# Kernel optimization log

Measured on AMD Instinct MI355X. Metric: run time of the kernel, lower is better.

## Reference

```python
import jax, jax.numpy as jnp
import numpy as np

C, Q, R, N, S = 10, 1000, 1024, 512, 10000
ALPHA, GAMMA, DIST_W, EPS_EYE = 0.25, 2.0, 0.1, 1e-4


def setup_inputs() -> dict:
    key = jax.random.key(0)
    ks = jax.random.split(key, 8)
    box_features = jax.random.normal(ks[0], (N, R), jnp.float32)
    id_labels = jax.random.randint(ks[1], (N,), 0, C, dtype=jnp.int32)
    id_data = jax.random.normal(ks[2], (C, Q, R), jnp.float32)
    id_data_counter = jnp.full((C,), Q, dtype=jnp.int32)  # full queues -> VOS path enabled
    W_pred = jax.random.normal(ks[3], (C, R), jnp.float32) * 0.02
    b_pred = jnp.zeros((C,), jnp.float32)
    w_e = jax.random.uniform(ks[4], (C, 1), jnp.float32)  # energy_score_weights ~ U[0,1)
    dist_W1 = jax.random.normal(ks[5], (512, 1), jnp.float32) * 0.5
    dist_b1 = jnp.zeros((512,), jnp.float32)
    dist_W2 = jax.random.normal(ks[6], (1, 512), jnp.float32) * 0.05
    dist_b2 = jnp.zeros((1,), jnp.float32)
    eps = jax.random.normal(ks[7], (C, S, R), jnp.float32)  # standard-normal draws for rsample
    return dict(box_features=box_features, id_labels=id_labels, id_data=id_data,
                id_data_counter=id_data_counter, W_pred=W_pred, b_pred=b_pred, w_e=w_e,
                dist_W1=dist_W1, dist_b1=dist_b1, dist_W2=dist_W2, dist_b2=dist_b2, eps=eps)


def _bce_logits(x, y):
    # binary_cross_entropy_with_logits, elementwise
    return jnp.maximum(x, 0.0) - x * y + jnp.log1p(jnp.exp(-jnp.abs(x)))


def _queue_update(id_data, counter, labels, feats):
    # Faithful sequential per-sample queue scatter (torch Python loop) as lax.scan.
    def step(carry, inp):
        data, cnt = carry
        lab, f = inp
        c = cnt[lab]
        row = data[lab]                                            # [Q,R]
        row_set = jax.lax.dynamic_update_slice(row, f[None], (c, 0))
        row_roll = jnp.concatenate([row[1:], f[None]], axis=0)     # drop oldest, append
        full = c >= row.shape[0]
        new_row = jnp.where(full, row_roll, row_set)
        data = data.at[lab].set(new_row)
        cnt = cnt.at[lab].add(jnp.where(full, 0, 1))
        return (data, cnt), None
    (data, cnt), _ = jax.lax.scan(step, (id_data, counter), (labels, feats))
    return data, cnt


def _energy(x, w_e):
    # m + log(exp(x-m) @ relu(w_e)); all classes valid (counter > 0)
    m = jnp.max(x, axis=1, keepdims=True)
    return m + jnp.log(jnp.exp(x - m) @ jax.nn.relu(w_e))


def reference(box_features, id_labels, id_data, id_data_counter, W_pred, b_pred, w_e,
              dist_W1, dist_b1, dist_W2, dist_b2, eps):
    scores = box_features @ W_pred.T + b_pred                      # [N,C]
    # ---- classification: sigmoid focal loss (sum / num_pos) ----
    t = jax.nn.one_hot(id_labels, C, dtype=scores.dtype)
    p = jax.nn.sigmoid(scores)
    ce = _bce_logits(scores, t)
    p_t = p * t + (1.0 - p) * (1.0 - t)
    alpha_t = ALPHA * t + (1.0 - ALPHA) * (1.0 - t)
    cls_loss = jnp.sum(alpha_t * ce * (1.0 - p_t) ** GAMMA) / scores.shape[0]
    # ---- per-class queue scatter (detached features) ----
    data, _ = _queue_update(id_data, id_data_counter, id_labels,
                            jax.lax.stop_gradient(box_features))
    # ---- class Gaussians: per-class mean, shared covariance ----
    mu = jnp.mean(data, axis=1)                                    # [C,R]
    x_tilda = (data - mu[:, None, :]).reshape(-1, R)               # all classes valid (full queues)
    sigma = x_tilda.T @ x_tilda / x_tilda.shape[0] + EPS_EYE * jnp.eye(R, dtype=data.dtype)
    L = jnp.linalg.cholesky(sigma)                                 # [R,R]
    # ---- VOS: rsample 10000 per class, keep lowest-density (top-1 of -log_prob) ----
    # samples = mu + eps @ L.T ; log_prob = const - 0.5*||eps||^2, so argmin density = argmax ||eps||^2
    sq = jnp.sum(eps * eps, axis=-1)                               # [C,S]
    idx = jnp.argmax(sq, axis=-1)                                  # [C]
    eps_sel = jnp.take_along_axis(eps, idx[:, None, None], axis=1)[:, 0, :]  # [C,R]
    vos_samples = mu + eps_sel @ L.T                               # [C,R]
    scores_vos = vos_samples @ W_pred.T + b_pred                   # [C,C]
    # ---- dist loss: energy score -> tiny MLP -> BCE, weight 0.1 ----
    e_all = jnp.concatenate([_energy(scores, w_e), _energy(scores_vos, w_e)], axis=0)  # [N+C,1]
    h = jax.nn.relu(e_all @ dist_W1.T + dist_b1)
    logits = (h @ dist_W2.T + dist_b2)[:, 0]                       # [N+C]
    y = jnp.concatenate([jnp.ones((scores.shape[0],), logits.dtype),
                         jnp.zeros((C,), logits.dtype)])
    dist_loss = DIST_W * jnp.mean(_bce_logits(logits, y))
    return cls_loss, dist_loss
```

## Files before the change

kernel.cpp:

```cpp
#include <hip/hip_runtime.h>
#include <hip/hip_cooperative_groups.h>
#include <stdint.h>

namespace cg = cooperative_groups;

#define C_ 10
#define Q_ 1000
#define R_ 1024
#define N_ 512
#define S_ 10000
#define CQ 10000
#define KP 10240
#define SPLITK 8
#define GRIDC 105

#define OFF_DT    0ULL
#define OFF_GP    20971520ULL
#define OFF_SIG   54525952ULL
#define OFF_MU    58720256ULL
#define OFF_E     58761216ULL
#define OFF_CLS   58763304ULL
#define OFF_AMAX  58763312ULL
#define OFF_KC    58763392ULL
#define OFF_GOFF  58763432ULL
#define OFF_GIDX  58763472ULL

typedef __attribute__((ext_vector_type(8))) short bf16x8;
typedef __attribute__((ext_vector_type(4))) float f32x4;

__global__ void k_prep(const int* __restrict__ labels, int* kc, int* goff, int* gidx,
                       float* mu, float* cls_accum, unsigned long long* amax) {
  __shared__ int cnt[C_];
  __shared__ int off[C_];
  int t = threadIdx.x;
  if (t < C_) cnt[t] = 0;
  __syncthreads();
  for (int i = t; i < N_; i += 256) atomicAdd(&cnt[labels[i]], 1);
  __syncthreads();
  if (t == 0) {
    int acc = 0;
    for (int c = 0; c < C_; c++) { off[c] = acc; goff[c] = acc; kc[c] = cnt[c]; acc += cnt[c]; }
    for (int i = 0; i < N_; i++) { int c = labels[i]; gidx[off[c]++] = i; }
    *cls_accum = 0.f;
  }
  if (t < C_) amax[t] = 0ULL;
  for (int i = t; i < C_ * R_; i += 256) mu[i] = 0.f;
}

__global__ __launch_bounds__(256) void k_epsmax(const float* __restrict__ eps,
                                                unsigned long long* amax) {
  int c = blockIdx.y;
  int chunk = blockIdx.x;
  int t = threadIdx.x, lane = t & 63, w = t >> 6;
  const int per = 79;
  int s0 = chunk * per;
  int s1 = min(s0 + per, S_);
  float bv = -1.f; int bs = 0;
  for (int s = s0 + w; s < s1; s += 4) {
    const float4* p = (const float4*)(eps + ((size_t)c * S_ + s) * R_);
    float acc = 0.f;
#pragma unroll
    for (int m = 0; m < 4; m++) {
      float4 v = p[lane + 64 * m];
      acc += v.x * v.x + v.y * v.y + v.z * v.z + v.w * v.w;
    }
#pragma unroll
    for (int d = 32; d > 0; d >>= 1) acc += __shfl_xor(acc, d);
    if (acc > bv) { bv = acc; bs = s; }
  }
  __shared__ float svv[4]; __shared__ int ssi[4];
  if (lane == 0) { svv[w] = bv; ssi[w] = bs; }
  __syncthreads();
  if (t == 0) {
    float m = svv[0]; int mi = ssi[0];
    for (int i = 1; i < 4; i++) if (svv[i] > m) { m = svv[i]; mi = ssi[i]; }
    if (m >= 0.f) {
      unsigned long long pk = ((unsigned long long)__float_as_uint(m) << 32) | (unsigned)mi;
      atomicMax(amax + c, pk);
    }
  }
}

__global__ void k_scores(const float* __restrict__ box, const int* __restrict__ labels,
                         const float* __restrict__ Wp, const float* __restrict__ bp,
                         const float* __restrict__ we, float* __restrict__ E,
                         float* cls_accum) {
  int i = blockIdx.x;
  int lane = threadIdx.x;
  float s[C_];
#pragma unroll
  for (int k = 0; k < C_; k++) s[k] = 0.f;
  const float* bi = box + (size_t)i * R_;
  for (int r = lane; r < R_; r += 64) {
    float x = bi[r];
#pragma unroll
    for (int k = 0; k < C_; k++) s[k] += x * Wp[k * R_ + r];
  }
#pragma unroll
  for (int k = 0; k < C_; k++) {
#pragma unroll
    for (int d = 32; d > 0; d >>= 1) s[k] += __shfl_xor(s[k], d);
  }
  if (lane == 0) {
    int lab = labels[i];
    float sc[C_]; float m = -1e30f;
#pragma unroll
    for (int k = 0; k < C_; k++) { sc[k] = s[k] + bp[k]; m = fmaxf(m, sc[k]); }
    float fsum = 0.f, esum = 0.f;
#pragma unroll
    for (int k = 0; k < C_; k++) {
      float x = sc[k];
      float tt = (k == lab) ? 1.f : 0.f;
      float p = 1.f / (1.f + expf(-x));
      float ce = fmaxf(x, 0.f) - x * tt + log1pf(expf(-fabsf(x)));
      float pt = p * tt + (1.f - p) * (1.f - tt);
      float at = 0.25f * tt + 0.75f * (1.f - tt);
      float om = 1.f - pt;
      fsum += at * ce * om * om;
      esum += expf(x - m) * fmaxf(we[k], 0.f);
    }
    atomicAdd(cls_accum, fsum);
    E[i] = m + logf(esum);
  }
}

__global__ __launch_bounds__(256) void k_convert(const float* __restrict__ idd,
                                                 const float* __restrict__ box,
                                                 const int* __restrict__ kc,
                                                 const int* __restrict__ goff,
                                                 const int* __restrict__ gidx,
                                                 uint16_t* __restrict__ Dt,
                                                 float* __restrict__ mu) {
  __shared__ const float* rowsrc[64];
  __shared__ int rcls[64];
  __shared__ float T[64][65];
  int bk = blockIdx.x;
  int br = blockIdx.y;
  int t = threadIdx.x;
  int t0 = bk * 64, r0 = br * 64;
  if (t < 64) {
    int row = t0 + t;
    const float* src = nullptr; int c = -1;
    if (row < CQ) {
      c = row / Q_;
      int q = row - c * Q_;
      int k = kc[c];
      if (q < Q_ - k) src = idd + (size_t)(c * Q_ + q + k) * R_;
      else            src = box + (size_t)gidx[goff[c] + (q - (Q_ - k))] * R_;
    }
    rowsrc[t] = src; rcls[t] = c;
  }
  __syncthreads();
  int rr = t & 63, k4 = t >> 6;
#pragma unroll
  for (int it = 0; it < 16; it++) {
    int kk = k4 + it * 4;
    const float* src = rowsrc[kk];
    T[kk][rr] = src ? src[r0 + rr] : 0.f;
  }
  __syncthreads();
  if (t < 64 && t0 < CQ) {
    int c0 = rcls[0];
    float s0 = 0.f, s1 = 0.f; int c1 = -1;
    for (int kk = 0; kk < 64; kk++) {
      int c = rcls[kk]; float v = T[kk][t];
      if (c == c0) s0 += v; else if (c >= 0) { c1 = c; s1 += v; }
    }
    atomicAdd(&mu[c0 * R_ + r0 + t], s0);
    if (c1 >= 0) atomicAdd(&mu[c1 * R_ + r0 + t], s1);
  }
  int kk2 = t & 63, r4 = t >> 6;
#pragma unroll
  for (int it = 0; it < 16; it++) {
    int rr2 = r4 + it * 4;
    float v = T[kk2][rr2];
    uint32_t u = __float_as_uint(v);
    uint32_t b = (u + 0x7fffu + ((u >> 16) & 1u)) >> 16;
    Dt[(size_t)(r0 + rr2) * KP + t0 + kk2] = (uint16_t)b;
  }
}

__global__ __launch_bounds__(256) void k_gemm(const uint16_t* __restrict__ Dt,
                                              float* __restrict__ GP) {
  __shared__ __align__(16) uint16_t lA[2][8192];
  __shared__ __align__(16) uint16_t lB[2][8192];
  int bi = blockIdx.x, bj = blockIdx.y, bz = blockIdx.z;
  int t = threadIdx.x;
  int lane = t & 63, w = t >> 6;
  int i0 = bi * 128, j0 = bj * 128;
  int lane16 = lane & 15, quad = lane >> 4;
  int wm = w >> 1, wn = w & 1;
  int row = t >> 1, half = t & 1;
  int kz = bz * 1280;
  const uint16_t* ga = Dt + (size_t)(i0 + row) * KP + kz + half * 32;
  const uint16_t* gb = Dt + (size_t)(j0 + row) * KP + kz + half * 32;
  int swz[4];
#pragma unroll
  for (int u = 0; u < 4; u++) swz[u] = (((half << 2) | u) ^ (row & 7)) << 3;
  int x7 = lane16 & 7;

  f32x4 acc[4][4];
#pragma unroll
  for (int a = 0; a < 4; a++)
#pragma unroll
    for (int b = 0; b < 4; b++) acc[a][b] = (f32x4){0.f, 0.f, 0.f, 0.f};

  uint4 ra[4], rb[4];
#pragma unroll
  for (int u = 0; u < 4; u++) {
    ra[u] = *(const uint4*)(ga + u * 8);
    rb[u] = *(const uint4*)(gb + u * 8);
  }
#pragma unroll
  for (int u = 0; u < 4; u++) {
    *(uint4*)(lA[0] + row * 64 + swz[u]) = ra[u];
    *(uint4*)(lB[0] + row * 64 + swz[u]) = rb[u];
  }
  __syncthreads();

  for (int it = 0; it < 20; it++) {
    int cur = it & 1;
    bool more = (it + 1) < 20;
    if (more) {
      const uint16_t* pa = ga + (it + 1) * 64;
      const uint16_t* pb = gb + (it + 1) * 64;
#pragma unroll
      for (int u = 0; u < 4; u++) {
        ra[u] = *(const uint4*)(pa + u * 8);
        rb[u] = *(const uint4*)(pb + u * 8);
      }
    }
#pragma unroll
    for (int ch = 0; ch < 2; ch++) {
      bf16x8 af[4], bfr[4];
#pragma unroll
      for (int mi = 0; mi < 4; mi++) {
        int r = wm * 64 + mi * 16 + lane16;
        int ck = ((ch << 2) | quad) ^ x7;
        af[mi] = *(const bf16x8*)(lA[cur] + r * 64 + ck * 8);
      }
#pragma unroll
      for (int ni = 0; ni < 4; ni++) {
        int r = wn * 64 + ni * 16 + lane16;
        int ck = ((ch << 2) | quad) ^ x7;
        bfr[ni] = *(const bf16x8*)(lB[cur] + r * 64 + ck * 8);
      }
#pragma unroll
      for (int mi = 0; mi < 4; mi++)
#pragma unroll
        for (int ni = 0; ni < 4; ni++)
          acc[mi][ni] = __builtin_amdgcn_mfma_f32_16x16x32_bf16(af[mi], bfr[ni], acc[mi][ni], 0, 0, 0);
    }
    if (more) {
      int nxt = cur ^ 1;
#pragma unroll
      for (int u = 0; u < 4; u++) {
        *(uint4*)(lA[nxt] + row * 64 + swz[u]) = ra[u];
        *(uint4*)(lB[nxt] + row * 64 + swz[u]) = rb[u];
      }
    }
    __syncthreads();
  }
  float* gp = GP + (size_t)bz * 1048576;
#pragma unroll
  for (int mi = 0; mi < 4; mi++)
#pragma unroll
    for (int ni = 0; ni < 4; ni++) {
      int col = j0 + wn * 64 + ni * 16 + lane16;
      int rowb = i0 + wm * 64 + mi * 16 + quad * 4;
#pragma unroll
      for (int r = 0; r < 4; r++)
        gp[(size_t)(rowb + r) * 1024 + col] = acc[mi][ni][r];
    }
}

__global__ void k_reduce(const float* __restrict__ GP, const float* __restrict__ mu,
                         float* __restrict__ sig) {
  int idx = blockIdx.x * 256 + threadIdx.x;
  int i = idx >> 10, j = idx & 1023;
  float g = 0.f;
#pragma unroll
  for (int s2 = 0; s2 < SPLITK; s2++) g += GP[idx + s2 * 1048576];
  float mm = 0.f;
#pragma unroll
  for (int c = 0; c < C_; c++) mm += mu[c * R_ + i] * mu[c * R_ + j];
  sig[idx] = g * 1e-4f - mm * 1e-7f + ((i == j) ? 1e-4f : 0.f);
}

#define AIDX(i, j) (((i) << 7) + (((j) + (i)) & 127))
__device__ void chol_diag_body(float* __restrict__ sig, int p, float* __restrict__ a) {
  int t = threadIdx.x;
  int base = p * 128;
  int lane = t & 63, wv = t >> 6;
  for (int idx = t; idx < 16384; idx += 256) {
    int i = idx >> 7, j = idx & 127;
    a[AIDX(i, j)] = sig[(size_t)(base + i) * 1024 + base + j];
  }
  __syncthreads();
  for (int panel = 0; panel < 8; panel++) {
    int j0 = panel * 16;
    if (wv == 0) {
      float pa0[16], pa1[16];
#pragma unroll
      for (int jj = 0; jj < 16; jj++) {
        pa0[jj] = a[AIDX(lane, j0 + jj)];
        pa1[jj] = a[AIDX(lane + 64, j0 + jj)];
      }
#pragma unroll
      for (int jj = 0; jj < 16; jj++) {
        int j = j0 + jj;
        float pv0 = __shfl(pa0[jj], j & 63);
        float pv1 = __shfl(pa1[jj], j & 63);
        float pv = (j < 64) ? pv0 : pv1;
// ... 40 lines not shown
          for (int n = 0; n < 4; n++) ak[n] = a[AIDX(gk + n, j0 + jj)];
#pragma unroll
          for (int m = 0; m < 4; m++)
#pragma unroll
            for (int n = 0; n < 4; n++) acc[m][n] += ai[m] * ak[n];
        }
#pragma unroll
        for (int m = 0; m < 4; m++)
#pragma unroll
          for (int n = 0; n < 4; n++)
            a[AIDX(gi + m, gk + n)] -= acc[m][n];
      }
    }
    __syncthreads();
  }
  for (int idx = t; idx < 16384; idx += 256) {
    int i = idx >> 7, j = idx & 127;
    sig[(size_t)(base + i) * 1024 + base + j] = a[AIDX(i, j)];
  }
}

#define XIDX(j, r) (((j) << 6) + (((r) + (j)) & 63))
__device__ void chol_trsm_body(float* __restrict__ sig, int p, int bid, float* __restrict__ smem) {
  float* Ls = smem;
  float* XT = smem + 8192;
  int t = threadIdx.x;
  int base = p * 128;
  int row0 = base + 128 + bid * 64;
  int r = t & 63, wv = t >> 6;
  for (int idx = t; idx < 8128; idx += 256) {
    int k = (int)((sqrtf(8.f * idx + 1.f) + 1.f) * 0.5f);
    while (k * (k - 1) / 2 > idx) k--;
    while ((k + 1) * k / 2 <= idx) k++;
    int j = idx - k * (k - 1) / 2;
    Ls[idx] = sig[(size_t)(base + k) * 1024 + base + j];
  }
  for (int idx = t; idx < 8192; idx += 256) {
    int rr = idx >> 7, j = idx & 127;
    XT[XIDX(j, rr)] = sig[(size_t)(row0 + rr) * 1024 + base + j];
  }
  float rd0 = 0.f, rd1 = 0.f;
  if (wv == 0) {
    rd0 = 1.0f / sig[(size_t)(base + r) * 1024 + base + r];
    rd1 = 1.0f / sig[(size_t)(base + 64 + r) * 1024 + base + 64 + r];
  }
  __syncthreads();
  for (int pb = 0; pb < 8; pb++) {
    int j0 = pb * 16;
    if (j0 > 0) {
      int c0 = j0 + wv * 4;
      int b0 = c0 * (c0 - 1) / 2, b1 = (c0 + 1) * c0 / 2;
      int b2 = (c0 + 2) * (c0 + 1) / 2, b3 = (c0 + 3) * (c0 + 2) / 2;
      float acc0 = 0.f, acc1 = 0.f, acc2 = 0.f, acc3 = 0.f;
      for (int k = 0; k < j0; k++) {
        float xk = XT[XIDX(k, r)];
        acc0 += xk * Ls[b0 + k];
        acc1 += xk * Ls[b1 + k];
        acc2 += xk * Ls[b2 + k];
        acc3 += xk * Ls[b3 + k];
      }
      XT[XIDX(c0 + 0, r)] -= acc0;
      XT[XIDX(c0 + 1, r)] -= acc1;
      XT[XIDX(c0 + 2, r)] -= acc2;
      XT[XIDX(c0 + 3, r)] -= acc3;
    }
    __syncthreads();
    if (wv == 0) {
#pragma unroll
      for (int jj = 0; jj < 16; jj++) {
        int j = j0 + jj;
        float rdj = (j < 64) ? __shfl(rd0, j & 63) : __shfl(rd1, j & 63);
        float xj = XT[XIDX(j, r)] * rdj;
        XT[XIDX(j, r)] = xj;
#pragma unroll
        for (int kk = jj + 1; kk < 16; kk++) {
          int k2 = j0 + kk;
          XT[XIDX(k2, r)] -= xj * Ls[k2 * (k2 - 1) / 2 + j];
        }
      }
    }
    __syncthreads();
  }
  for (int idx = t; idx < 8192; idx += 256) {
    int rr = idx >> 7, j = idx & 127;
    sig[(size_t)(row0 + rr) * 1024 + base + j] = XT[XIDX(j, rr)];
  }
}

__device__ void chol_syrk_body(float* __restrict__ sig, int p, int bid, float* __restrict__ smem) {
  float (*PA)[65] = (float(*)[65])smem;
  float (*PB)[65] = (float(*)[65])(smem + 4160);
  int t = threadIdx.x;
  int tb = p * 128 + 128;
  int I = 0;
  while ((I + 1) * (I + 2) / 2 <= bid) I++;
  int K = bid - I * (I + 1) / 2;
  int gi = tb + I * 64, gk = tb + K * 64;
  int a4 = t >> 4, b4 = t & 15;
  float acc[4][4];
#pragma unroll
  for (int m = 0; m < 4; m++)
#pragma unroll
    for (int n = 0; n < 4; n++) acc[m][n] = 0.f;
  for (int ch = 0; ch < 2; ch++) {
    int cb = p * 128 + ch * 64;
    for (int idx = t; idx < 4096; idx += 256) {
      int rr = idx >> 6, cc = idx & 63;
      PA[rr][cc] = sig[(size_t)(gi + rr) * 1024 + cb + cc];
      PB[rr][cc] = sig[(size_t)(gk + rr) * 1024 + cb + cc];
    }
    __syncthreads();
    for (int j = 0; j < 64; j++) {
      float pa[4], pb[4];
#pragma unroll
      for (int m = 0; m < 4; m++) pa[m] = PA[a4 * 4 + m][j];
#pragma unroll
      for (int n = 0; n < 4; n++) pb[n] = PB[b4 * 4 + n][j];
#pragma unroll
      for (int m = 0; m < 4; m++)
#pragma unroll
        for (int n = 0; n < 4; n++) acc[m][n] += pa[m] * pb[n];
    }
    __syncthreads();
  }
#pragma unroll
  for (int m = 0; m < 4; m++)
#pragma unroll
    for (int n = 0; n < 4; n++)
      sig[(size_t)(gi + a4 * 4 + m) * 1024 + gk + b4 * 4 + n] -= acc[m][n];
}

__device__ void vos_body(const float* __restrict__ eps, const float* __restrict__ L,
                         const float* __restrict__ mu, const float* __restrict__ Wp,
                         const float* __restrict__ bp, const float* __restrict__ we,
                         const unsigned long long* __restrict__ amax,
                         float* __restrict__ E, int c, float* __restrict__ smem) {
  float* es = smem;
  float* ys = smem + 1024;
  float* sv = smem + 2048;
  int t = threadIdx.x;
  int idx = (int)(amax[c] & 0xffffffffULL);
  for (int i = t; i < 1024; i += 256) es[i] = eps[((size_t)c * S_ + idx) * R_ + i];
  __syncthreads();
  for (int rep = 0; rep < 4; rep++) {
    int i = rep * 256 + t;
    const float* Lr = L + (size_t)i * 1024;
    float a0 = 0.f, a1 = 0.f, a2 = 0.f, a3 = 0.f;
    int j = 0;
    for (; j + 3 <= i; j += 4) {
      a0 += es[j] * Lr[j];
      a1 += es[j + 1] * Lr[j + 1];
      a2 += es[j + 2] * Lr[j + 2];
      a3 += es[j + 3] * Lr[j + 3];
    }
    for (; j <= i; j++) a0 += es[j] * Lr[j];
    ys[i] = mu[c * R_ + i] * 1e-3f + ((a0 + a1) + (a2 + a3));
  }
  __syncthreads();
  if (t < C_) {
    float acc = bp[t];
    const float* Wr = Wp + (size_t)t * R_;
    for (int j = 0; j < 1024; j++) acc += ys[j] * Wr[j];
    sv[t] = acc;
  }
  __syncthreads();
  if (t == 0) {
    float m = -1e30f;
    for (int k = 0; k < C_; k++) m = fmaxf(m, sv[k]);
    float sum = 0.f;
    for (int k = 0; k < C_; k++) sum += expf(sv[k] - m) * fmaxf(we[k], 0.f);
    E[N_ + c] = m + logf(sum);
  }
}

__device__ void dist_body(const float* __restrict__ E, const float* __restrict__ W1,
                          const float* __restrict__ b1, const float* __restrict__ W2,
                          const float* __restrict__ b2, const float* __restrict__ cls_accum,
                          float* __restrict__ out, float* __restrict__ smem) {
  float* sW1 = smem;
  float* sb1 = smem + 512;
  float* sW2 = smem + 1024;
  float* red = smem + 1536;
  int t = threadIdx.x;
  for (int i = t; i < 512; i += 256) { sW1[i] = W1[i]; sb1[i] = b1[i]; sW2[i] = W2[i]; }
  __syncthreads();
  float sum = 0.f;
  for (int i = t; i < N_ + C_; i += 256) {
    float e = E[i];
    float acc = b2[0];
    for (int j = 0; j < 512; j++) acc += sW2[j] * fmaxf(e * sW1[j] + sb1[j], 0.f);
    float y = (i < N_) ? 1.f : 0.f;
    float l = fmaxf(acc, 0.f) - acc * y + log1pf(expf(-fabsf(acc)));
    sum += l;
  }
#pragma unroll
  for (int d = 32; d > 0; d >>= 1) sum += __shfl_xor(sum, d);
  if ((t & 63) == 0) red[t >> 6] = sum;
  __syncthreads();
  if (t == 0) {
    out[1] = 0.1f * (red[0] + red[1] + red[2] + red[3]) / 522.f;
    out[0] = *cls_accum / 512.f;
  }
}

__global__ __launch_bounds__(256) void k_chol(float* __restrict__ sig,
    const float* __restrict__ eps, const float* __restrict__ mu,
    const float* __restrict__ Wp, const float* __restrict__ bp,
    const float* __restrict__ we, const unsigned long long* __restrict__ amax,
    float* __restrict__ E, const float* __restrict__ W1, const float* __restrict__ b1,
    const float* __restrict__ W2, const float* __restrict__ b2,
    const float* __restrict__ cls_accum, float* __restrict__ out) {
  cg::grid_group grid = cg::this_grid();
  __shared__ __align__(16) float smem[16384];
  int bid = blockIdx.x;
  for (int p = 0; p < 8; p++) {
    if (bid == 0) chol_diag_body(sig, p, smem);
    __threadfence(); grid.sync();
    int rows = 1024 - 128 * (p + 1);
    if (rows > 0) {
      int nb = rows >> 6;
      if (bid < nb) chol_trsm_body(sig, p, bid, smem);
      __threadfence(); grid.sync();
      int nt = nb * (nb + 1) / 2;
      for (int bx = bid; bx < nt; bx += GRIDC) chol_syrk_body(sig, p, bx, smem);
      __threadfence(); grid.sync();
    }
  }
  if (bid < C_) vos_body(eps, sig, mu, Wp, bp, we, amax, E, bid, smem);
  __threadfence(); grid.sync();
  if (bid == 0) dist_body(E, W1, b1, W2, b2, cls_accum, out, smem);
}

extern "C" void kernel_launch(void* const* d_in, const int* in_sizes, int n_in,
                              void* d_out, int out_size, void* d_ws, size_t ws_size,
                              hipStream_t stream) {
  (void)in_sizes; (void)n_in; (void)out_size; (void)ws_size;
  const float* box  = (const float*)d_in[0];
  const int*   lab  = (const int*)d_in[1];
  const float* idd  = (const float*)d_in[2];
  const float* Wp   = (const float*)d_in[4];
  const float* bp   = (const float*)d_in[5];
  const float* we   = (const float*)d_in[6];
  const float* W1   = (const float*)d_in[7];
  const float* b1   = (const float*)d_in[8];
  const float* W2   = (const float*)d_in[9];
  const float* b2   = (const float*)d_in[10];
  const float* eps  = (const float*)d_in[11];
  float* out = (float*)d_out;

  char* ws = (char*)d_ws;
  uint16_t* Dt = (uint16_t*)(ws + OFF_DT);
  float* GP    = (float*)(ws + OFF_GP);
  float* sig   = (float*)(ws + OFF_SIG);
  float* mu    = (float*)(ws + OFF_MU);
  float* E     = (float*)(ws + OFF_E);
  float* clsa  = (float*)(ws + OFF_CLS);
  unsigned long long* amax = (unsigned long long*)(ws + OFF_AMAX);
  int* kc   = (int*)(ws + OFF_KC);
  int* goff = (int*)(ws + OFF_GOFF);
  int* gidx = (int*)(ws + OFF_GIDX);

  hipLaunchKernelGGL(k_prep, dim3(1), dim3(256), 0, stream, lab, kc, goff, gidx, mu, clsa, amax);
  hipLaunchKernelGGL(k_epsmax, dim3(127, C_), dim3(256), 0, stream, eps, amax);
  hipLaunchKernelGGL(k_scores, dim3(N_), dim3(64), 0, stream, box, lab, Wp, bp, we, E, clsa);
  hipLaunchKernelGGL(k_convert, dim3(160, 16), dim3(256), 0, stream, idd, box, kc, goff, gidx, Dt, mu);
  hipLaunchKernelGGL(k_gemm, dim3(8, 8, SPLITK), dim3(256), 0, stream, Dt, GP);
  hipLaunchKernelGGL(k_reduce, dim3(4096), dim3(256), 0, stream, GP, mu, sig);
  {
    float* a0 = sig; const float* a1 = eps; const float* a2 = mu; const float* a3 = Wp;
    const float* a4 = bp; const float* a5 = we; const unsigned long long* a6 = amax;
    float* a7 = E; const float* a8 = W1; const float* a9 = b1; const float* a10 = W2;
    const float* a11 = b2; const float* a12 = clsa; float* a13 = out;
    void* args[] = {&a0, &a1, &a2, &a3, &a4, &a5, &a6, &a7, &a8, &a9, &a10, &a11, &a12, &a13};
    hipLaunchCooperativeKernel(k_chol, dim3(GRIDC), dim3(256), args, 0, stream);
  }
}
```

Measured before the change: 2.515 ms.

## Replace cooperative Cholesky with per-panel launches and fuse front-end kernels

Merges the prep, eps argmax, score and convert kernels into one launch, with a memset taking over the zero-initialisation. The cooperative Cholesky with grid syncs is replaced by per-panel fused TRSM+SYRK launches. The last-arriving block, detected via an atomic counter, factors the next diagonal block, and the first diagonal factor is triggered from the GEMM. The split-K reduction and covariance correction are folded lazily into the Cholesky reads, and VOS plus the distance loss become one kernel that uses a last-block pattern. This removes grid-wide barriers and several launches, but adds redundant per-block label scans and recomputation of triangular solves per tile.

Result: slower. 3.081 ms (+22.5%).

```diff
diff --git a/kernel.cpp b/kernel.cpp
--- a/kernel.cpp
+++ b/kernel.cpp
@@ -1,8 +1,5 @@
 #include <hip/hip_runtime.h>
-#include <hip/hip_cooperative_groups.h>
 #include <stdint.h>
-
-namespace cg = cooperative_groups;
 
 #define C_ 10
 #define Q_ 1000
@@ -12,7 +9,7 @@
 #define CQ 10000
 #define KP 10240
 #define SPLITK 8
-#define GRIDC 105
+#define GPN 1048576
 
 #define OFF_DT    0ULL
 #define OFF_GP    20971520ULL
@@ -21,132 +18,127 @@
 #define OFF_E     58761216ULL
 #define OFF_CLS   58763304ULL
 #define OFF_AMAX  58763312ULL
-#define OFF_KC    58763392ULL
-#define OFF_GOFF  58763432ULL
-#define OFF_GIDX  58763472ULL
+#define OFF_CNT   58763392ULL
+#define ZERO_BYTES 43200ULL
 
 typedef __attribute__((ext_vector_type(8))) short bf16x8;
 typedef __attribute__((ext_vector_type(4))) float f32x4;
 
-__global__ void k_prep(const int* __restrict__ labels, int* kc, int* goff, int* gidx,
-                       float* mu, float* cls_accum, unsigned long long* amax) {
-  __shared__ int cnt[C_];
-  __shared__ int off[C_];
-  int t = threadIdx.x;
-  if (t < C_) cnt[t] = 0;
-  __syncthreads();
-  for (int i = t; i < N_; i += 256) atomicAdd(&cnt[labels[i]], 1);
-  __syncthreads();
-  if (t == 0) {
-    int acc = 0;
-    for (int c = 0; c < C_; c++) { off[c] = acc; goff[c] = acc; kc[c] = cnt[c]; acc += cnt[c]; }
-    for (int i = 0; i < N_; i++) { int c = labels[i]; gidx[off[c]++] = i; }
-    *cls_accum = 0.f;
-  }
-  if (t < C_) amax[t] = 0ULL;
-  for (int i = t; i < C_ * R_; i += 256) mu[i] = 0.f;
-}
-
-__global__ __launch_bounds__(256) void k_epsmax(const float* __restrict__ eps,
-                                                unsigned long long* amax) {
-  int c = blockIdx.y;
-  int chunk = blockIdx.x;
-  int t = threadIdx.x, lane = t & 63, w = t >> 6;
-  const int per = 79;
-  int s0 = chunk * per;
-  int s1 = min(s0 + per, S_);
-  float bv = -1.f; int bs = 0;
-  for (int s = s0 + w; s < s1; s += 4) {
-    const float4* p = (const float4*)(eps + ((size_t)c * S_ + s) * R_);
-    float acc = 0.f;
-#pragma unroll
-    for (int m = 0; m < 4; m++) {
-      float4 v = p[lane + 64 * m];
-      acc += v.x * v.x + v.y * v.y + v.z * v.z + v.w * v.w;
-    }
-#pragma unroll
-    for (int d = 32; d > 0; d >>= 1) acc += __shfl_xor(acc, d);
-    if (acc > bv) { bv = acc; bs = s; }
-  }
-  __shared__ float svv[4]; __shared__ int ssi[4];
-  if (lane == 0) { svv[w] = bv; ssi[w] = bs; }
-  __syncthreads();
-  if (t == 0) {
-    float m = svv[0]; int mi = ssi[0];
-    for (int i = 1; i < 4; i++) if (svv[i] > m) { m = svv[i]; mi = ssi[i]; }
-    if (m >= 0.f) {
-      unsigned long long pk = ((unsigned long long)__float_as_uint(m) << 32) | (unsigned)mi;
-      atomicMax(amax + c, pk);
-    }
-  }
-}
-
-__global__ void k_scores(const float* __restrict__ box, const int* __restrict__ labels,
-                         const float* __restrict__ Wp, const float* __restrict__ bp,
-                         const float* __restrict__ we, float* __restrict__ E,
-                         float* cls_accum) {
-  int i = blockIdx.x;
-  int lane = threadIdx.x;
-  float s[C_];
-#pragma unroll
-  for (int k = 0; k < C_; k++) s[k] = 0.f;
-  const float* bi = box + (size_t)i * R_;
-  for (int r = lane; r < R_; r += 64) {
-    float x = bi[r];
-#pragma unroll
-    for (int k = 0; k < C_; k++) s[k] += x * Wp[k * R_ + r];
-  }
-#pragma unroll
-  for (int k = 0; k < C_; k++) {
-#pragma unroll
-    for (int d = 32; d > 0; d >>= 1) s[k] += __shfl_xor(s[k], d);
-  }
-  if (lane == 0) {
-    int lab = labels[i];
-    float sc[C_]; float m = -1e30f;
-#pragma unroll
-    for (int k = 0; k < C_; k++) { sc[k] = s[k] + bp[k]; m = fmaxf(m, sc[k]); }
-    float fsum = 0.f, esum = 0.f;
-#pragma unroll
-    for (int k = 0; k < C_; k++) {
-      float x = sc[k];
-      float tt = (k == lab) ? 1.f : 0.f;
-      float p = 1.f / (1.f + expf(-x));
-      float ce = fmaxf(x, 0.f) - x * tt + log1pf(expf(-fabsf(x)));
-      float pt = p * tt + (1.f - p) * (1.f - tt);
-      float at = 0.25f * tt + 0.75f * (1.f - tt);
-      float om = 1.f - pt;
-      fsum += at * ce * om * om;
-      esum += expf(x - m) * fmaxf(we[k], 0.f);
-    }
-    atomicAdd(cls_accum, fsum);
-    E[i] = m + logf(esum);
-  }
-}
-
-__global__ __launch_bounds__(256) void k_convert(const float* __restrict__ idd,
-                                                 const float* __restrict__ box,
-                                                 const int* __restrict__ kc,
-                                                 const int* __restrict__ goff,
-                                                 const int* __restrict__ gidx,
-                                                 uint16_t* __restrict__ Dt,
-                                                 float* __restrict__ mu) {
+#define AIDX(i, j) (((i) << 7) + (((j) + (i)) & 127))
+#define XIDX(j, r) (((j) << 6) + (((r) + (j)) & 63))
+
+__global__ __launch_bounds__(256) void k_front(
+    const float* __restrict__ box, const int* __restrict__ labels,
+    const float* __restrict__ idd, const float* __restrict__ Wp,
+    const float* __restrict__ bp, const float* __restrict__ we,
+    const float* __restrict__ eps, uint16_t* __restrict__ Dt,
+    float* __restrict__ mu, float* __restrict__ E, float* cls_accum,
+    unsigned long long* amax) {
   __shared__ const float* rowsrc[64];
   __shared__ int rcls[64];
   __shared__ float T[64][65];
-  int bk = blockIdx.x;
-  int br = blockIdx.y;
+  __shared__ int s_cnt[C_];
+  __shared__ float svv[4];
+  __shared__ int ssi[4];
+  int b = blockIdx.x;
   int t = threadIdx.x;
+
+  if (b < 1270) {
+    int c = b / 127, chunk = b % 127;
+    int lane = t & 63, w = t >> 6;
+    const int per = 79;
+    int s0 = chunk * per;
+    int s1 = min(s0 + per, S_);
+    float bv = -1.f; int bs = 0;
+    for (int s = s0 + w; s < s1; s += 4) {
+      const float4* p = (const float4*)(eps + ((size_t)c * S_ + s) * R_);
+      float acc = 0.f;
+#pragma unroll
+      for (int m = 0; m < 4; m++) {
+        float4 v = p[lane + 64 * m];
+        acc += v.x * v.x + v.y * v.y + v.z * v.z + v.w * v.w;
+      }
+#pragma unroll
+      for (int d = 32; d > 0; d >>= 1) acc += __shfl_xor(acc, d);
+      if (acc > bv) { bv = acc; bs = s; }
+    }
+    if (lane == 0) { svv[w] = bv; ssi[w] = bs; }
+    __syncthreads();
+    if (t == 0) {
+      float m = svv[0]; int mi = ssi[0];
+      for (int i = 1; i < 4; i++) if (svv[i] > m) { m = svv[i]; mi = ssi[i]; }
+      if (m >= 0.f) {
+        unsigned long long pk = ((unsigned long long)__float_as_uint(m) << 32) | (unsigned)mi;
+        atomicMax(amax + c, pk);
+      }
+    }
+    return;
+  }
+
+  if (b < 1270 + 128) {
+    int lane = t & 63, wv = t >> 6;
+    int i = (b - 1270) * 4 + wv;
+    float s[C_];
+#pragma unroll
+    for (int k = 0; k < C_; k++) s[k] = 0.f;
+    const float* bi = box + (size_t)i * R_;
+    for (int r = lane; r < R_; r += 64) {
+      float x = bi[r];
+#pragma unroll
+      for (int k = 0; k < C_; k++) s[k] += x * Wp[k * R_ + r];
+    }
+#pragma unroll
+    for (int k = 0; k < C_; k++) {
+#pragma unroll
+      for (int d = 32; d > 0; d >>= 1) s[k] += __shfl_xor(s[k], d);
+    }
+    if (lane == 0) {
+      int lab = labels[i];
+      float sc[C_]; float m = -1e30f;
+#pragma unroll
+      for (int k = 0; k < C_; k++) { sc[k] = s[k] + bp[k]; m = fmaxf(m, sc[k]); }
+      float fsum = 0.f, esum = 0.f;
+#pragma unroll
+      for (int k = 0; k < C_; k++) {
+        float x = sc[k];
+        float tt = (k == lab) ? 1.f : 0.f;
+        float p = 1.f / (1.f + expf(-x));
+        float ce = fmaxf(x, 0.f) - x * tt + log1pf(expf(-fabsf(x)));
+        float pt = p * tt + (1.f - p) * (1.f - tt);
+        float at = 0.25f * tt + 0.75f * (1.f - tt);
+        float om = 1.f - pt;
+        fsum += at * ce * om * om;
+        esum += expf(x - m) * fmaxf(we[k], 0.f);
+      }
+      atomicAdd(cls_accum, fsum);
+      E[i] = m + logf(esum);
+    }
+    return;
+  }
+
+  int cb = b - 1398;
+  int bk = cb % 160, br = cb / 160;
   int t0 = bk * 64, r0 = br * 64;
+  if (t < C_) s_cnt[t] = 0;
+  __syncthreads();
+  for (int i = t; i < N_; i += 256) atomicAdd(&s_cnt[labels[i]], 1);
+  __syncthreads();
   if (t < 64) {
     int row = t0 + t;
     const float* src = nullptr; int c = -1;
     if (row < CQ) {
       c = row / Q_;
       int q = row - c * Q_;
-      int k = kc[c];
+      int k = s_cnt[c];
       if (q < Q_ - k) src = idd + (size_t)(c * Q_ + q + k) * R_;
-      else            src = box + (size_t)gidx[goff[c] + (q - (Q_ - k))] * R_;
+      else {
+        int m = q - (Q_ - k);
+        int cnt2 = 0, gi2 = 0;
+        for (int i2 = 0; i2 < N_; i2++) {
+          if (labels[i2] == c) { if (cnt2 == m) { gi2 = i2; break; } cnt2++; }
+        }
+        src = box + (size_t)gi2 * R_;
+      }
     }
     rowsrc[t] = src; rcls[t] = c;
   }
@@ -175,128 +167,14 @@
     int rr2 = r4 + it * 4;
     float v = T[kk2][rr2];
     uint32_t u = __float_as_uint(v);
-    uint32_t b = (u + 0x7fffu + ((u >> 16) & 1u)) >> 16;
-    Dt[(size_t)(r0 + rr2) * KP + t0 + kk2] = (uint16_t)b;
-  }
-}
-
-__global__ __launch_bounds__(256) void k_gemm(const uint16_t* __restrict__ Dt,
-                                              float* __restrict__ GP) {
-  __shared__ __align__(16) uint16_t lA[2][8192];
-  __shared__ __align__(16) uint16_t lB[2][8192];
-  int bi = blockIdx.x, bj = blockIdx.y, bz = blockIdx.z;
+    uint32_t bb = (u + 0x7fffu + ((u >> 16) & 1u)) >> 16;
+    Dt[(size_t)(r0 + rr2) * KP + t0 + kk2] = (uint16_t)bb;
+  }
+}
+
+__device__ void diag_factor(float* __restrict__ a) {
   int t = threadIdx.x;
-  int lane = t & 63, w = t >> 6;
-  int i0 = bi * 128, j0 = bj * 128;
-  int lane16 = lane & 15, quad = lane >> 4;
-  int wm = w >> 1, wn = w & 1;
-  int row = t >> 1, half = t & 1;
-  int kz = bz * 1280;
-  const uint16_t* ga = Dt + (size_t)(i0 + row) * KP + kz + half * 32;
-  const uint16_t* gb = Dt + (size_t)(j0 + row) * KP + kz + half * 32;
-  int swz[4];
-#pragma unroll
-  for (int u = 0; u < 4; u++) swz[u] = (((half << 2) | u) ^ (row & 7)) << 3;
-  int x7 = lane16 & 7;
-
-  f32x4 acc[4][4];
-#pragma unroll
-  for (int a = 0; a < 4; a++)
-#pragma unroll
-    for (int b = 0; b < 4; b++) acc[a][b] = (f32x4){0.f, 0.f, 0.f, 0.f};
-
-  uint4 ra[4], rb[4];
-#pragma unroll
-  for (int u = 0; u < 4; u++) {
-    ra[u] = *(const uint4*)(ga + u * 8);
-    rb[u] = *(const uint4*)(gb + u * 8);
-  }
-#pragma unroll
-  for (int u = 0; u < 4; u++) {
-    *(uint4*)(lA[0] + row * 64 + swz[u]) = ra[u];
-    *(uint4*)(lB[0] + row * 64 + swz[u]) = rb[u];
-  }
-  __syncthreads();
-
-  for (int it = 0; it < 20; it++) {
-    int cur = it & 1;
-    bool more = (it + 1) < 20;
-    if (more) {
-      const uint16_t* pa = ga + (it + 1) * 64;
-      const uint16_t* pb = gb + (it + 1) * 64;
-#pragma unroll
-      for (int u = 0; u < 4; u++) {
-        ra[u] = *(const uint4*)(pa + u * 8);
-        rb[u] = *(const uint4*)(pb + u * 8);
-      }
-    }
-#pragma unroll
-    for (int ch = 0; ch < 2; ch++) {
-      bf16x8 af[4], bfr[4];
-#pragma unroll
-      for (int mi = 0; mi < 4; mi++) {
-        int r = wm * 64 + mi * 16 + lane16;
-        int ck = ((ch << 2) | quad) ^ x7;
-        af[mi] = *(const bf16x8*)(lA[cur] + r * 64 + ck * 8);
-      }
-#pragma unroll
-      for (int ni = 0; ni < 4; ni++) {
-        int r = wn * 64 + ni * 16 + lane16;
-        int ck = ((ch << 2) | quad) ^ x7;
-        bfr[ni] = *(const bf16x8*)(lB[cur] + r * 64 + ck * 8);
-      }
-#pragma unroll
-      for (int mi = 0; mi < 4; mi++)
-#pragma unroll
-        for (int ni = 0; ni < 4; ni++)
-          acc[mi][ni] = __builtin_amdgcn_mfma_f32_16x16x32_bf16(af[mi], bfr[ni], acc[mi][ni], 0, 0, 0);
-    }
-    if (more) {
-      int nxt = cur ^ 1;
-#pragma unroll
-      for (int u = 0; u < 4; u++) {
-        *(uint4*)(lA[nxt] + row * 64 + swz[u]) = ra[u];
-        *(uint4*)(lB[nxt] + row * 64 + swz[u]) = rb[u];
-      }
-    }
-    __syncthreads();
-  }
-  float* gp = GP + (size_t)bz * 1048576;
-#pragma unroll
-  for (int mi = 0; mi < 4; mi++)
-#pragma unroll
-    for (int ni = 0; ni < 4; ni++) {
-      int col = j0 + wn * 64 + ni * 16 + lane16;
-      int rowb = i0 + wm * 64 + mi * 16 + quad * 4;
-#pragma unroll
-      for (int r = 0; r < 4; r++)
-        gp[(size_t)(rowb + r) * 1024 + col] = acc[mi][ni][r];
-    }
-}
-
-__global__ void k_reduce(const float* __restrict__ GP, const float* __restrict__ mu,
-                         float* __restrict__ sig) {
-  int idx = blockIdx.x * 256 + threadIdx.x;
-  int i = idx >> 10, j = idx & 1023;
-  float g = 0.f;
-#pragma unroll
-  for (int s2 = 0; s2 < SPLITK; s2++) g += GP[idx + s2 * 1048576];
-  float mm = 0.f;
-#pragma unroll
-  for (int c = 0; c < C_; c++) mm += mu[c * R_ + i] * mu[c * R_ + j];
-  sig[idx] = g * 1e-4f - mm * 1e-7f + ((i == j) ? 1e-4f : 0.f);
-}
-
-#define AIDX(i, j) (((i) << 7) + (((j) + (i)) & 127))
-__device__ void chol_diag_body(float* __restrict__ sig, int p, float* __restrict__ a) {
-  int t = threadIdx.x;
-  int base = p * 128;
   int lane = t & 63, wv = t >> 6;
-  for (int idx = t; idx < 16384; idx += 256) {
-    int i = idx >> 7, j = idx & 127;
-    a[AIDX(i, j)] = sig[(size_t)(base + i) * 1024 + base + j];
-  }
-  __syncthreads();
   for (int panel = 0; panel < 8; panel++) {
     int j0 = panel * 16;
     if (wv == 0) {
@@ -367,147 +245,317 @@
     }
     __syncthreads();
   }
+}
+
+__device__ __forceinline__ float sig_corr(const float* __restrict__ GP,
+                                          const float* __restrict__ mu,
+                                          int i, int j) {
+  size_t o = (size_t)i * 1024 + j;
+  float g = 0.f;
+#pragma unroll
+  for (int s = 0; s < SPLITK; s++) g += GP[(size_t)s * GPN + o];
+  float mm = 0.f;
+#pragma unroll
+  for (int c = 0; c < C_; c++) mm += mu[c * R_ + i] * mu[c * R_ + j];
+  return g * 1e-4f - mm * 1e-7f + ((i == j) ? 1e-4f : 0.f);
+}
+
+__device__ void diag_tail(float* __restrict__ sig, const float* __restrict__ GP,
+                          const float* __restrict__ mu, int p, int fromGP,
+                          float* __restrict__ a) {
+  int t = threadIdx.x;
+  int base = p * 128;
+  for (int idx = t; idx < 16384; idx += 256) {
+    int i = idx >> 7, j = idx & 127;
+    float v = 0.f;
+    if (j <= i) {
+      if (fromGP) v = sig_corr(GP, mu, base + i, base + j);
+      else        v = sig[(size_t)(base + i) * 1024 + base + j];
+    }
+    a[AIDX(i, j)] = v;
+  }
+  __syncthreads();
+  diag_factor(a);
   for (int idx = t; idx < 16384; idx += 256) {
     int i = idx >> 7, j = idx & 127;
     sig[(size_t)(base + i) * 1024 + base + j] = a[AIDX(i, j)];
   }
 }
 
-#define XIDX(j, r) (((j) << 6) + (((r) + (j)) & 63))
-__device__ void chol_trsm_body(float* __restrict__ sig, int p, int bid, float* __restrict__ smem) {
-  float* Ls = smem;
-  float* XT = smem + 8192;
+__device__ void solve_panel(const float* __restrict__ sig, const float* __restrict__ GP,
+                            const float* __restrict__ mu, int base, int grow,
+                            int fromGP, float* __restrict__ XT, float rd0, float rd1) {
+  int t = threadIdx.x;
+  int r = t & 63, wv = t >> 6;
+  for (int idx = t; idx < 8192; idx += 256) {
+    int rr = idx >> 7, j = idx & 127;
+    int gi = grow + rr, gj = base + j;
+    float v;
+    if (fromGP) v = sig_corr(GP, mu, gi, gj);
+    else        v = sig[(size_t)gi * 1024 + gj];
+    XT[XIDX(j, rr)] = v;
+  }
+  __syncthreads();
+  const float* L00 = sig + (size_t)base * 1024 + base;
+  for (int pb = 0; pb < 8; pb++) {
+    int j0 = pb * 16;
+    if (j0 > 0) {
+      int c0 = j0 + wv * 4;
+      const float* l0 = L00 + (size_t)c0 * 1024;
+      float acc0 = 0.f, acc1 = 0.f, acc2 = 0.f, acc3 = 0.f;
+      for (int k = 0; k < j0; k++) {
+        float xk = XT[XIDX(k, r)];
+        acc0 += xk * l0[k];
+        acc1 += xk * l0[1024 + k];
+        acc2 += xk * l0[2048 + k];
+        acc3 += xk * l0[3072 + k];
+      }
+      XT[XIDX(c0 + 0, r)] -= acc0;
+      XT[XIDX(c0 + 1, r)] -= acc1;
+      XT[XIDX(c0 + 2, r)] -= acc2;
+      XT[XIDX(c0 + 3, r)] -= acc3;
+    }
+    __syncthreads();
+    if (wv == 0) {
+#pragma unroll
+      for (int jj = 0; jj < 16; jj++) {
+        int j = j0 + jj;
+        float rdj = (j < 64) ? __shfl(rd0, j) : __shfl(rd1, j - 64);
+        float xj = XT[XIDX(j, r)] * rdj;
+        XT[XIDX(j, r)] = xj;
+#pragma unroll
+        for (int kk = jj + 1; kk < 16; kk++) {
+          int k2 = j0 + kk;
+          XT[XIDX(k2, r)] -= xj * L00[(size_t)k2 * 1024 + j];
+        }
+      }
+    }
+    __syncthreads();
+  }
+}
+
+__global__ __launch_bounds__(256) void k_gemm(const uint16_t* __restrict__ Dt,
+                                              float* __restrict__ GP,
+                                              const float* __restrict__ mu,
+                                              float* __restrict__ sig,
+                                              int* __restrict__ cnt) {
+  __shared__ __align__(16) union SM {
+    struct { uint16_t A[2][8192]; uint16_t B[2][8192]; } g;
+    float a[16384];
+  } sm;
+  int bi = blockIdx.x, bj = blockIdx.y, bz = blockIdx.z;
+  int t = threadIdx.x;
+  int lane = t & 63, w = t >> 6;
+  int i0 = bi * 128, j0 = bj * 128;
+  int lane16 = lane & 15, quad = lane >> 4;
+  int wm = w >> 1, wn = w & 1;
+  int row = t >> 1, half = t & 1;
+  int kz = bz * 1280;
+  const uint16_t* ga = Dt + (size_t)(i0 + row) * KP + kz + half * 32;
+  const uint16_t* gb = Dt + (size_t)(j0 + row) * KP + kz + half * 32;
+  int swz[4];
+#pragma unroll
+  for (int u = 0; u < 4; u++) swz[u] = (((half << 2) | u) ^ (row & 7)) << 3;
+  int x7 = lane16 & 7;
+
+  f32x4 acc[4][4];
+#pragma unroll
+  for (int a = 0; a < 4; a++)
+#pragma unroll
+    for (int b = 0; b < 4; b++) acc[a][b] = (f32x4){0.f, 0.f, 0.f, 0.f};
+
+  uint4 ra[4], rb[4];
+#pragma unroll
+  for (int u = 0; u < 4; u++) {
+    ra[u] = *(const uint4*)(ga + u * 8);
+    rb[u] = *(const uint4*)(gb + u * 8);
+  }
+#pragma unroll
+  for (int u = 0; u < 4; u++) {
+    *(uint4*)(sm.g.A[0] + row * 64 + swz[u]) = ra[u];
+    *(uint4*)(sm.g.B[0] + row * 64 + swz[u]) = rb[u];
+  }
+  __syncthreads();
+
+  for (int it = 0; it < 20; it++) {
+    int cur = it & 1;
+    bool more = (it + 1) < 20;
+    if (more) {
+      const uint16_t* pa = ga + (it + 1) * 64;
+      const uint16_t* pb = gb + (it + 1) * 64;
+#pragma unroll
+      for (int u = 0; u < 4; u++) {
+        ra[u] = *(const uint4*)(pa + u * 8);
+        rb[u] = *(const uint4*)(pb + u * 8);
+      }
+    }
+#pragma unroll
+    for (int ch = 0; ch < 2; ch++) {
+      bf16x8 af[4], bfr[4];
+#pragma unroll
+      for (int mi = 0; mi < 4; mi++) {
+        int rr = wm * 64 + mi * 16 + lane16;
+        int ck = ((ch << 2) | quad) ^ x7;
+        af[mi] = *(const bf16x8*)(sm.g.A[cur] + rr * 64 + ck * 8);
+      }
+#pragma unroll
+      for (int ni = 0; ni < 4; ni++) {
+        int rr = wn * 64 + ni * 16 + lane16;
+        int ck = ((ch << 2) | quad) ^ x7;
+        bfr[ni] = *(const bf16x8*)(sm.g.B[cur] + rr * 64 + ck * 8);
+      }
+#pragma unroll
+      for (int mi = 0; mi < 4; mi++)
+#pragma unroll
+        for (int ni = 0; ni < 4; ni++)
+          acc[mi][ni] = __builtin_amdgcn_mfma_f32_16x16x32_bf16(af[mi], bfr[ni], acc[mi][ni], 0, 0, 0);
+    }
+    if (more) {
+      int nxt = cur ^ 1;
+#pragma unroll
+      for (int u = 0; u < 4; u++) {
+        *(uint4*)(sm.g.A[nxt] + row * 64 + swz[u]) = ra[u];
+        *(uint4*)(sm.g.B[nxt] + row * 64 + swz[u]) = rb[u];
+      }
+    }
+    __syncthreads();
+  }
+  float* gp = GP + (size_t)bz * GPN;
+#pragma unroll
+  for (int mi = 0; mi < 4; mi++)
+#pragma unroll
+    for (int ni = 0; ni < 4; ni++) {
+      int col = j0 + wn * 64 + ni * 16 + lane16;
+      int rowb = i0 + wm * 64 + mi * 16 + quad * 4;
+#pragma unroll
+      for (int r = 0; r < 4; r++)
+        gp[(size_t)(rowb + r) * 1024 + col] = acc[mi][ni][r];
+    }
+  __syncthreads();
+  if (t == 0) {
+    __threadfence();
+    int d = atomicAdd(&cnt[8], 1);
+    sm.a[0] = (d == 511) ? 1.f : 0.f;
+  }
+  __syncthreads();
+  bool last = (sm.a[0] != 0.f);
+  __syncthreads();
+  if (!last) return;
+  __threadfence();
+  diag_tail(sig, GP, mu, 0, 1, sm.a);
+}
+
+__global__ __launch_bounds__(256) void k_tsyrk(float* __restrict__ sig,
+                                               float* __restrict__ GP,
+                                               const float* __restrict__ mu,
+                                               int* __restrict__ cnt,
+                                               int p, int nt) {
+  __shared__ __align__(16) float arena[16384];
+  float* XI = arena;
+  float* XK = arena + 8192;
   int t = threadIdx.x;
   int base = p * 128;
-  int row0 = base + 128 + bid * 64;
+  int bid = blockIdx.x;
+  int I = 0;
+  while ((I + 1) * (I + 2) / 2 <= bid) I++;
+  int K = bid - I * (I + 1) / 2;
+  int gi = base + 128 + I * 64, gk = base + 128 + K * 64;
   int r = t & 63, wv = t >> 6;
-  for (int idx = t; idx < 8128; idx += 256) {
-    int k = (int)((sqrtf(8.f * idx + 1.f) + 1.f) * 0.5f);
-    while (k * (k - 1) / 2 > idx) k--;
-    while ((k + 1) * k / 2 <= idx) k++;
-    int j = idx - k * (k - 1) / 2;
-    Ls[idx] = sig[(size_t)(base + k) * 1024 + base + j];
-  }
-  for (int idx = t; idx < 8192; idx += 256) {
-    int rr = idx >> 7, j = idx & 127;
-    XT[XIDX(j, rr)] = sig[(size_t)(row0 + rr) * 1024 + base + j];
-  }
   float rd0 = 0.f, rd1 = 0.f;
   if (wv == 0) {
     rd0 = 1.0f / sig[(size_t)(base + r) * 1024 + base + r];
     rd1 = 1.0f / sig[(size_t)(base + 64 + r) * 1024 + base + 64 + r];
   }
-  __syncthreads();
-  for (int pb = 0; pb < 8; pb++) {
-    int j0 = pb * 16;
-    if (j0 > 0) {
-      int c0 = j0 + wv * 4;
-      int b0 = c0 * (c0 - 1) / 2, b1 = (c0 + 1) * c0 / 2;
-      int b2 = (c0 + 2) * (c0 + 1) / 2, b3 = (c0 + 3) * (c0 + 2) / 2;
-      float acc0 = 0.f, acc1 = 0.f, acc2 = 0.f, acc3 = 0.f;
-      for (int k = 0; k < j0; k++) {
-        float xk = XT[XIDX(k, r)];
-        acc0 += xk * Ls[b0 + k];
-        acc1 += xk * Ls[b1 + k];
-        acc2 += xk * Ls[b2 + k];
-        acc3 += xk * Ls[b3 + k];
-      }
-      XT[XIDX(c0 + 0, r)] -= acc0;
-      XT[XIDX(c0 + 1, r)] -= acc1;
-      XT[XIDX(c0 + 2, r)] -= acc2;
-      XT[XIDX(c0 + 3, r)] -= acc3;
-    }
-    __syncthreads();
-    if (wv == 0) {
-#pragma unroll
-      for (int jj = 0; jj < 16; jj++) {
-        int j = j0 + jj;
-        float rdj = (j < 64) ? __shfl(rd0, j & 63) : __shfl(rd1, j & 63);
-        float xj = XT[XIDX(j, r)] * rdj;
-        XT[XIDX(j, r)] = xj;
-#pragma unroll
-        for (int kk = jj + 1; kk < 16; kk++) {
-          int k2 = j0 + kk;
-          XT[XIDX(k2, r)] -= xj * Ls[k2 * (k2 - 1) / 2 + j];
-        }
-      }
-    }
-    __syncthreads();
-  }
-  for (int idx = t; idx < 8192; idx += 256) {
-    int rr = idx >> 7, j = idx & 127;
-    sig[(size_t)(row0 + rr) * 1024 + base + j] = XT[XIDX(j, rr)];
-  }
-}
-
-__device__ void chol_syrk_body(float* __restrict__ sig, int p, int bid, float* __restrict__ smem) {
-  float (*PA)[65] = (float(*)[65])smem;
-  float (*PB)[65] = (float(*)[65])(smem + 4160);
-  int t = threadIdx.x;
-  int tb = p * 128 + 128;
-  int I = 0;
-  while ((I + 1) * (I + 2) / 2 <= bid) I++;
-  int K = bid - I * (I + 1) / 2;
-  int gi = tb + I * 64, gk = tb + K * 64;
+  int fromGP = (p == 0);
+  solve_panel(sig, GP, mu, base, gi, fromGP, XI, rd0, rd1);
+  if (I != K) solve_panel(sig, GP, mu, base, gk, fromGP, XK, rd0, rd1);
+  if (I == K) {
+    if (p == 0) {
+      for (int idx = t; idx < 8192; idx += 256) {
+        int rr = idx >> 7, j = idx & 127;
+        sig[(size_t)(gi + rr) * 1024 + j] = XI[XIDX(j, rr)];
+      }
+    } else {
+      float* xb = GP + (size_t)(p - 1) * 114688;
+      for (int idx = t; idx < 8192; idx += 256) {
+        int rr = idx >> 7, j = idx & 127;
+        xb[(size_t)(I * 64 + rr) * 128 + j] = XI[XIDX(j, rr)];
+      }
+    }
+  }
+  const float* XKp = (I == K) ? XI : XK;
   int a4 = t >> 4, b4 = t & 15;
   float acc[4][4];
 #pragma unroll
   for (int m = 0; m < 4; m++)
 #pragma unroll
     for (int n = 0; n < 4; n++) acc[m][n] = 0.f;
-  for (int ch = 0; ch < 2; ch++) {
-    int cb = p * 128 + ch * 64;
-    for (int idx = t; idx < 4096; idx += 256) {
-      int rr = idx >> 6, cc = idx & 63;
-      PA[rr][cc] = sig[(size_t)(gi + rr) * 1024 + cb + cc];
-      PB[rr][cc] = sig[(size_t)(gk + rr) * 1024 + cb + cc];
-    }
-    __syncthreads();
-    for (int j = 0; j < 64; j++) {
-      float pa[4], pb[4];
-#pragma unroll
-      for (int m = 0; m < 4; m++) pa[m] = PA[a4 * 4 + m][j];
-#pragma unroll
-      for (int n = 0; n < 4; n++) pb[n] = PB[b4 * 4 + n][j];
-#pragma unroll
-      for (int m = 0; m < 4; m++)
-#pragma unroll
-        for (int n = 0; n < 4; n++) acc[m][n] += pa[m] * pb[n];
-    }
-    __syncthreads();
+  for (int j = 0; j < 128; j++) {
+    float pa[4], pb[4];
+#pragma unroll
+    for (int m = 0; m < 4; m++) pa[m] = XI[XIDX(j, a4 * 4 + m)];
+#pragma unroll
+    for (int n = 0; n < 4; n++) pb[n] = XKp[XIDX(j, b4 * 4 + n)];
+#pragma unroll
+    for (int m = 0; m < 4; m++)
+#pragma unroll
+      for (int n = 0; n < 4; n++) acc[m][n] += pa[m] * pb[n];
   }
 #pragma unroll
   for (int m = 0; m < 4; m++)
 #pragma unroll
-    for (int n = 0; n < 4; n++)
-      sig[(size_t)(gi + a4 * 4 + m) * 1024 + gk + b4 * 4 + n] -= acc[m][n];
-}
-
-__device__ void vos_body(const float* __restrict__ eps, const float* __restrict__ L,
-                         const float* __restrict__ mu, const float* __restrict__ Wp,
-                         const float* __restrict__ bp, const float* __restrict__ we,
-                         const unsigned long long* __restrict__ amax,
-                         float* __restrict__ E, int c, float* __restrict__ smem) {
-  float* es = smem;
-  float* ys = smem + 1024;
-  float* sv = smem + 2048;
-  int t = threadIdx.x;
+    for (int n = 0; n < 4; n++) {
+      int ii = gi + a4 * 4 + m, jj = gk + b4 * 4 + n;
+      size_t o = (size_t)ii * 1024 + jj;
+      float v = fromGP ? sig_corr(GP, mu, ii, jj) : sig[o];
+      sig[o] = v - acc[m][n];
+    }
+  __syncthreads();
+  if (t == 0) {
+    __threadfence();
+    int d = atomicAdd(&cnt[p], 1);
+    arena[0] = (d == nt - 1) ? 1.f : 0.f;
+  }
+  __syncthreads();
+  bool last = (arena[0] != 0.f);
+  __syncthreads();
+  if (!last) return;
+  __threadfence();
+  diag_tail(sig, GP, mu, p + 1, 0, arena);
+}
+
+__global__ __launch_bounds__(256) void k_vosdist(
+    const float* __restrict__ eps, const float* __restrict__ sig,
+    const float* __restrict__ XB, const float* __restrict__ mu,
+    const float* __restrict__ Wp, const float* __restrict__ bp,
+    const float* __restrict__ we, const unsigned long long* __restrict__ amax,
+    float* __restrict__ E, const float* __restrict__ W1,
+    const float* __restrict__ b1, const float* __restrict__ W2,
+    const float* __restrict__ b2, const float* __restrict__ cls_accum,
+    float* __restrict__ out, int* __restrict__ cnt) {
+  __shared__ float es[1024];
+  __shared__ float ys[1024];
+  __shared__ float sv[16];
+  __shared__ float darena[1540];
+  __shared__ int lastf;
+  int c = blockIdx.x, t = threadIdx.x;
   int idx = (int)(amax[c] & 0xffffffffULL);
   for (int i = t; i < 1024; i += 256) es[i] = eps[((size_t)c * S_ + idx) * R_ + i];
   __syncthreads();
   for (int rep = 0; rep < 4; rep++) {
     int i = rep * 256 + t;
-    const float* Lr = L + (size_t)i * 1024;
-    float a0 = 0.f, a1 = 0.f, a2 = 0.f, a3 = 0.f;
-    int j = 0;
-    for (; j + 3 <= i; j += 4) {
-      a0 += es[j] * Lr[j];
-      a1 += es[j + 1] * Lr[j + 1];
-      a2 += es[j + 2] * Lr[j + 2];
-      a3 += es[j + 3] * Lr[j + 3];
-    }
-    for (; j <= i; j++) a0 += es[j] * Lr[j];
-    ys[i] = mu[c * R_ + i] * 1e-3f + ((a0 + a1) + (a2 + a3));
+    int q = i >> 7;
+    float acc = 0.f;
+    for (int pp = 0; pp < q; pp++) {
+      const float* xr = (pp == 0) ? (sig + (size_t)i * 1024)
+                                  : (XB + (size_t)(pp - 1) * 114688 + (size_t)(i - 128 * (pp + 1)) * 128);
+      const float* ev = es + 128 * pp;
+#pragma unroll 4
+      for (int j = 0; j < 128; j++) acc += xr[j] * ev[j];
+    }
+    const float* dr = sig + (size_t)i * 1024;
+    for (int j = 128 * q; j <= i; j++) acc += dr[j] * es[j];
+    ys[i] = mu[c * R_ + i] * 1e-3f + acc;
   }
   __syncthreads();
   if (t < C_) {
@@ -523,18 +571,17 @@
     float sum = 0.f;
     for (int k = 0; k < C_; k++) sum += expf(sv[k] - m) * fmaxf(we[k], 0.f);
     E[N_ + c] = m + logf(sum);
-  }
-}
-
-__device__ void dist_body(const float* __restrict__ E, const float* __restrict__ W1,
-                          const float* __restrict__ b1, const float* __restrict__ W2,
-                          const float* __restrict__ b2, const float* __restrict__ cls_accum,
-                          float* __restrict__ out, float* __restrict__ smem) {
-  float* sW1 = smem;
-  float* sb1 = smem + 512;
-  float* sW2 = smem + 1024;
-  float* red = smem + 1536;
-  int t = threadIdx.x;
+    __threadfence();
+    int d = atomicAdd(&cnt[9], 1);
+    lastf = (d == C_ - 1) ? 1 : 0;
+  }
+  __syncthreads();
+  if (!lastf) return;
+  __threadfence();
+  float* sW1 = darena;
+  float* sb1 = darena + 512;
+  float* sW2 = darena + 1024;
+  float* red = darena + 1536;
   for (int i = t; i < 512; i += 256) { sW1[i] = W1[i]; sb1[i] = b1[i]; sW2[i] = W2[i]; }
   __syncthreads();
   float sum = 0.f;
@@ -554,34 +601,6 @@
     out[1] = 0.1f * (red[0] + red[1] + red[2] + red[3]) / 522.f;
     out[0] = *cls_accum / 512.f;
   }
-}
-
-__global__ __launch_bounds__(256) void k_chol(float* __restrict__ sig,
-    const float* __restrict__ eps, const float* __restrict__ mu,
-    const float* __restrict__ Wp, const float* __restrict__ bp,
-    const float* __restrict__ we, const unsigned long long* __restrict__ amax,
-    float* __restrict__ E, const float* __restrict__ W1, const float* __restrict__ b1,
-    const float* __restrict__ W2, const float* __restrict__ b2,
-    const float* __restrict__ cls_accum, float* __restrict__ out) {
-  cg::grid_group grid = cg::this_grid();
-  __shared__ __align__(16) float smem[16384];
-  int bid = blockIdx.x;
-  for (int p = 0; p < 8; p++) {
-    if (bid == 0) chol_diag_body(sig, p, smem);
-    __threadfence(); grid.sync();
-    int rows = 1024 - 128 * (p + 1);
-    if (rows > 0) {
-      int nb = rows >> 6;
-      if (bid < nb) chol_trsm_body(sig, p, bid, smem);
-      __threadfence(); grid.sync();
-      int nt = nb * (nb + 1) / 2;
-      for (int bx = bid; bx < nt; bx += GRIDC) chol_syrk_body(sig, p, bx, smem);
-      __threadfence(); grid.sync();
-    }
-  }
-  if (bid < C_) vos_body(eps, sig, mu, Wp, bp, we, amax, E, bid, smem);
-  __threadfence(); grid.sync();
-  if (bid == 0) dist_body(E, W1, b1, W2, b2, cls_accum, out, smem);
 }
 
 extern "C" void kernel_launch(void* const* d_in, const int* in_sizes, int n_in,
@@ -609,22 +628,20 @@
   float* E     = (float*)(ws + OFF_E);
   float* clsa  = (float*)(ws + OFF_CLS);
   unsigned long long* amax = (unsigned long long*)(ws + OFF_AMAX);
-  int* kc   = (int*)(ws + OFF_KC);
-  int* goff = (int*)(ws + OFF_GOFF);
-  int* gidx = (int*)(ws + OFF_GIDX);
-
-  hipLaunchKernelGGL(k_prep, dim3(1), dim3(256), 0, stream, lab, kc, goff, gidx, mu, clsa, amax);
-  hipLaunchKernelGGL(k_epsmax, dim3(127, C_), dim3(256), 0, stream, eps, amax);
-  hipLaunchKernelGGL(k_scores, dim3(N_), dim3(64), 0, stream, box, lab, Wp, bp, we, E, clsa);
-  hipLaunchKernelGGL(k_convert, dim3(160, 16), dim3(256), 0, stream, idd, box, kc, goff, gidx, Dt, mu);
-  hipLaunchKernelGGL(k_gemm, dim3(8, 8, SPLITK), dim3(256), 0, stream, Dt, GP);
-  hipLaunchKernelGGL(k_reduce, dim3(4096), dim3(256), 0, stream, GP, mu, sig);
-  {
-    float* a0 = sig; const float* a1 = eps; const float* a2 = mu; const float* a3 = Wp;
-    const float* a4 = bp; const float* a5 = we; const unsigned long long* a6 = amax;
-    float* a7 = E; const float* a8 = W1; const float* a9 = b1; const float* a10 = W2;
-    const float* a11 = b2; const float* a12 = clsa; float* a13 = out;
-    void* args[] = {&a0, &a1, &a2, &a3, &a4, &a5, &a6, &a7, &a8, &a9, &a10, &a11, &a12, &a13};
-    hipLaunchCooperativeKernel(k_chol, dim3(GRIDC), dim3(256), args, 0, stream);
-  }
-}
+  int* cnt  = (int*)(ws + OFF_CNT);
+
+  hipMemsetAsync(ws + OFF_MU, 0, ZERO_BYTES, stream);
+  hipLaunchKernelGGL(k_front, dim3(3958), dim3(256), 0, stream,
+                     box, lab, idd, Wp, bp, we, eps, Dt, mu, E, clsa, amax);
+  hipLaunchKernelGGL(k_gemm, dim3(8, 8, SPLITK), dim3(256), 0, stream,
+                     Dt, GP, mu, sig, cnt);
+  for (int p = 0; p < 7; p++) {
+    int nb = 14 - 2 * p;
+    int nt = nb * (nb + 1) / 2;
+    hipLaunchKernelGGL(k_tsyrk, dim3(nt), dim3(256), 0, stream,
+                       sig, GP, mu, cnt, p, nt);
+  }
+  hipLaunchKernelGGL(k_vosdist, dim3(C_), dim3(256), 0, stream,
+                     eps, sig, GP, mu, Wp, bp, we, amax, E,
+                     W1, b1, W2, b2, clsa, out, cnt);
+}
```
